# Optimization experiments

Measured on AMD Instinct MI355X. Metric: run time of the kernel, lower is better.

## Reference

```python
import jax, jax.numpy as jnp
import numpy as np

B, X, Y, Z, C = 1, 16, 16, 16, 768
NUM_HEADS = 12


def setup_inputs() -> dict:
    key = jax.random.key(0)
    k0, k1, k2 = jax.random.split(key, 3)
    x = jax.random.normal(k0, (B, X, Y, Z, C), dtype=jnp.float32)
    # Linear weights stored as [in, out] (torch stores [out, in]; math is x @ W_in_out + b)
    w_qkv = jax.random.normal(k1, (C, 3 * C), dtype=jnp.float32) * 0.02
    b_qkv = jnp.zeros((3 * C,), dtype=jnp.float32)
    w_proj = jax.random.normal(k2, (C, C), dtype=jnp.float32) * 0.02
    b_proj = jnp.zeros((C,), dtype=jnp.float32)
    return {"x": x, "w_qkv": w_qkv, "b_qkv": b_qkv, "w_proj": w_proj, "b_proj": b_proj}


def reference(x, w_qkv, b_qkv, w_proj, b_proj):
    b, xx, yy, zz, c = x.shape
    h = NUM_HEADS
    hd = c // h
    scale = hd ** (-0.5)
    n = xx * yy * zz  # flatten 3D grid into tokens

    qkv = x.reshape(b, n, c) @ w_qkv + b_qkv          # [B, N, 3C]
    qkv = qkv.reshape(b, n, 3, h, hd).transpose(2, 0, 3, 1, 4)  # [3, B, H, N, hd]
    q, k, v = qkv[0], qkv[1], qkv[2]

    attn = jnp.einsum('bhnd,bhmd->bhnm', q * scale, k)  # [B, H, N, N]
    attn = jax.nn.softmax(attn, axis=-1)
    out = jnp.einsum('bhnm,bhmd->bhnd', attn, v)        # [B, H, N, hd]
    out = out.transpose(0, 2, 1, 3).reshape(b, n, c)
    out = out @ w_proj + b_proj
    return out.reshape(b, xx, yy, zz, c)
```

## Files before the change

### kernel.cpp

```cpp
#include <hip/hip_runtime.h>
#include <cstddef>

#define N_TOK 4096
#define C_DIM 768
#define H_NUM 12
#define C3    2304
#define NSPLIT 2

typedef unsigned short u16;
using short8  = __attribute__((ext_vector_type(8))) short;
using floatx4 = __attribute__((ext_vector_type(4))) float;
using u16x4   = __attribute__((ext_vector_type(4))) u16;
using uint4v  = __attribute__((ext_vector_type(4))) unsigned;

#define K2SCALE 0.18033688011112043f

__device__ __forceinline__ u16 f2bf(float f) {
  union { float f; unsigned u; } v; v.f = f;
  unsigned r = v.u + 0x7FFFu + ((v.u >> 16) & 1u);
  return (u16)(r >> 16);
}

__device__ __forceinline__ unsigned permpack(float a, float b) {
  union { float f; unsigned u; } x, y; x.f = a; y.f = b;
  return __builtin_amdgcn_perm(y.u, x.u, 0x07060302u);
}

__device__ __forceinline__ float aexp2(float x) {
  float r;
  asm("v_exp_f32 %0, %1" : "=v"(r) : "v"(x));
  return r;
}

__device__ __forceinline__ float arcp(float x) {
  float r;
  asm("v_rcp_f32 %0, %1" : "=v"(r) : "v"(x));
  return r;
}

__device__ __forceinline__ void pl_swap32(unsigned &a, unsigned &b) {
#if __has_builtin(__builtin_amdgcn_permlane32_swap)
  auto r = __builtin_amdgcn_permlane32_swap(a, b, false, false);
  a = r[0]; b = r[1];
#else
  asm("v_permlane32_swap_b32 %0, %1" : "+v"(a), "+v"(b));
#endif
}
__device__ __forceinline__ void pl_swap16(unsigned &a, unsigned &b) {
#if __has_builtin(__builtin_amdgcn_permlane16_swap)
  auto r = __builtin_amdgcn_permlane16_swap(a, b, false, false);
  a = r[0]; b = r[1];
#else
  asm("v_permlane16_swap_b32 %0, %1" : "+v"(a), "+v"(b));
#endif
}

__device__ __forceinline__ void gload_lds16(const void* g, void* l) {
  __builtin_amdgcn_global_load_lds(
      (const __attribute__((address_space(1))) unsigned int*)g,
      (__attribute__((address_space(3))) unsigned int*)l, 16, 0, 0);
}

__global__ void k_pre(const float* __restrict__ x, u16* __restrict__ xb,
                      const float* __restrict__ wq, u16* __restrict__ wqT,
                      const float* __restrict__ wp, u16* __restrict__ wpT,
                      float* __restrict__ Oz) {
  __shared__ float tile[32][33];
  const int b = blockIdx.x;
  if (b >= 5376) {
    size_t i = (size_t)(b - 5376) * 256 + threadIdx.x;
    float4 z; z.x = 0.f; z.y = 0.f; z.z = 0.f; z.w = 0.f;
    ((float4*)Oz)[i] = z;
    return;
  }
  if (b < 3072) {
    int i = b * 256 + threadIdx.x;
    float4 f = ((const float4*)x)[i];
    u16x4 o;
    o[0] = f2bf(f.x); o[1] = f2bf(f.y); o[2] = f2bf(f.z); o[3] = f2bf(f.w);
    ((u16x4*)xb)[i] = o;
    return;
  }
  const float* in; u16* out; int Cc, bx, by;
  if (b < 4800) { int t = b - 3072; in = wq; out = wqT; Cc = 2304; bx = t % 72; by = t / 72; }
  else          { int t = b - 4800; in = wp; out = wpT; Cc = 768;  bx = t % 24; by = t / 24; }
  const int R = 768;
  const int tx = threadIdx.x & 31;
  const int ty = threadIdx.x >> 5;
  const int c0 = bx * 32, r0 = by * 32;
#pragma unroll
  for (int i = 0; i < 32; i += 8)
    tile[ty + i][tx] = in[(size_t)(r0 + ty + i) * Cc + c0 + tx];
  __syncthreads();
#pragma unroll
  for (int i = 0; i < 32; i += 8)
    out[(size_t)(c0 + ty + i) * R + r0 + tx] = f2bf(tile[tx][ty + i]);
}

__global__ __launch_bounds__(256)
void k_gemm_qkv(const u16* __restrict__ A, const u16* __restrict__ B,
                const float* __restrict__ bias, u16* __restrict__ qkv,
                u16* __restrict__ vT) {
  __shared__ u16 As[2][128 * 32];
  __shared__ u16 Bs[2][128 * 32];
  const int K = C_DIM;
  const int tid  = threadIdx.x;
  const int wave = tid >> 6, lane = tid & 63, quad = lane >> 4, l16 = lane & 15;
  const int wrow = wave >> 1, wcol = wave & 1;
  const int bm = blockIdx.y, bn = blockIdx.x;
  const int r3 = l16 & 3;

  floatx4 acc[4][4];
#pragma unroll
  for (int i = 0; i < 4; ++i)
#pragma unroll
    for (int j = 0; j < 4; ++j)
#pragma unroll
      for (int r = 0; r < 4; ++r) acc[i][j][r] = 0.f;

  const int ar = tid >> 2;
  const int ac = ((tid & 3) ^ (ar & 3)) * 8;
  const u16* gA = A + (size_t)(bm * 128 + ar) * K + ac;
  const u16* gB = B + (size_t)(bn * 128 + ar) * K + ac;

  auto stage = [&](int b, int k0) {
    gload_lds16(gA + k0,                  &As[b][tid * 8]);
    gload_lds16(gA + k0 + (size_t)64 * K, &As[b][tid * 8 + 2048]);
    gload_lds16(gB + k0,                  &Bs[b][tid * 8]);
    gload_lds16(gB + k0 + (size_t)64 * K, &Bs[b][tid * 8 + 2048]);
  };

  stage(0, 0);
  __syncthreads();
  int buf = 0;
  for (int k0 = 0; k0 < K; k0 += 32) {
    if (k0 + 32 < K) stage(buf ^ 1, k0 + 32);
    short8 af[4], bf[4];
#pragma unroll
    for (int t = 0; t < 4; ++t) {
      af[t] = *(const short8*)&As[buf][(wrow * 64 + t * 16 + l16) * 32 + ((quad ^ r3) * 8)];
      bf[t] = *(const short8*)&Bs[buf][(wcol * 64 + t * 16 + l16) * 32 + ((quad ^ r3) * 8)];
    }
#pragma unroll
    for (int tm = 0; tm < 4; ++tm)
#pragma unroll
      for (int tn = 0; tn < 4; ++tn)
        acc[tm][tn] = __builtin_amdgcn_mfma_f32_16x16x32_bf16(af[tm], bf[tn], acc[tm][tn], 0, 0, 0);
    __syncthreads();
    buf ^= 1;
  }

  const float qs = (bn < 6) ? K2SCALE : 1.0f;
#pragma unroll
  for (int tn = 0; tn < 4; ++tn) {
    const int col = bn * 128 + wcol * 64 + tn * 16 + l16;
    const float bc = bias[col];
    if (col < 1536) {
#pragma unroll
      for (int tm = 0; tm < 4; ++tm) {
        const int rowb = bm * 128 + wrow * 64 + tm * 16 + quad * 4;
#pragma unroll
        for (int r = 0; r < 4; ++r)
          qkv[(size_t)(rowb + r) * C3 + col] = f2bf((acc[tm][tn][r] + bc) * qs);
      }
    } else {
      const int hd_ = col - 1536;
#pragma unroll
      for (int tm = 0; tm < 4; ++tm) {
        const int rowb = bm * 128 + wrow * 64 + tm * 16 + quad * 4;
        u16x4 pk;
#pragma unroll
        for (int r = 0; r < 4; ++r) pk[r] = f2bf(acc[tm][tn][r] + bc);
        *(u16x4*)&vT[(size_t)hd_ * N_TOK + rowb] = pk;
      }
    }
  }
}

__global__ __launch_bounds__(256, 3)
void k_flash(const u16* __restrict__ qkv, const u16* __restrict__ vT,
             float* __restrict__ Opart, float* __restrict__ lpart) {
  __shared__ u16 Ks[2][64 * 64];
  __shared__ u16 Vs[2][64 * 64];
  const int tid  = threadIdx.x;
  const int wave = tid >> 6, lane = tid & 63, quad = lane >> 4, l16 = lane & 15;
  const int h = blockIdx.x >> 1, split = blockIdx.x & 1, qt = blockIdx.y;
  const int lr = tid >> 3;
  const int lc = ((tid & 7) ^ (lr & 7)) * 8;
  const int r7 = l16 & 7;
  const int kb = split * 2048;

  short8 bq[2][2];
#pragma unroll
  for (int qs = 0; qs < 2; ++qs)
#pragma unroll
    for (int ks = 0; ks < 2; ++ks)
      bq[qs][ks] = *(const short8*)&qkv[(size_t)(qt * 128 + wave * 32 + qs * 16 + l16) * C3
                                        + h * 64 + ks * 32 + quad * 8];

  const u16* gk = qkv + (size_t)lr * C3 + C_DIM + h * 64 + lc;
  const u16* gv = vT + (size_t)(h * 64 + lr) * N_TOK + lc;

  auto stage = [&](int b, int m0) {
#pragma unroll
    for (int p = 0; p < 2; ++p) {
      gload_lds16(gk + (size_t)(m0 + p * 32) * C3,    &Ks[b][p * 2048 + tid * 8]);
      gload_lds16(gv + (size_t)(p * 32) * N_TOK + m0, &Vs[b][p * 2048 + tid * 8]);
    }
  };

  floatx4 o0[4], o1[4], l0, l1, zv;
#pragma unroll
  for (int r = 0; r < 4; ++r) { zv[r] = 0.f; l0[r] = 0.f; l1[r] = 0.f; }
#pragma unroll
  for (int d = 0; d < 4; ++d)
#pragma unroll
    for (int r = 0; r < 4; ++r) { o0[d][r] = 0.f; o1[d][r] = 0.f; }

  short8 ones;
#pragma unroll
  for (int i = 0; i < 8; ++i) ones[i] = (short)0x3F80;

  auto compute = [&](int b) __attribute__((always_inline)) {
    const u16* kbp = &Ks[b][0];
    const u16* vb  = &Vs[b][0];
    floatx4 s0[4], s1[4];
    __builtin_amdgcn_s_setprio(1);
#pragma unroll
    for (int tn = 0; tn < 4; ++tn) {
      short8 ak = *(const short8*)&kbp[(tn * 16 + l16) * 64 + (quad ^ r7) * 8];
      s0[tn] = __builtin_amdgcn_mfma_f32_16x16x32_bf16(ak, bq[0][0], zv, 0, 0, 0);
      s1[tn] = __builtin_amdgcn_mfma_f32_16x16x32_bf16(ak, bq[1][0], zv, 0, 0, 0);
    }
#pragma unroll
    for (int tn = 0; tn < 4; ++tn) {
      short8 ak = *(const short8*)&kbp[(tn * 16 + l16) * 64 + ((quad + 4) ^ r7) * 8];
      s0[tn] = __builtin_amdgcn_mfma_f32_16x16x32_bf16(ak, bq[0][1], s0[tn], 0, 0, 0);
      s1[tn] = __builtin_amdgcn_mfma_f32_16x16x32_bf16(ak, bq[1][1], s1[tn], 0, 0, 0);
    }
    __builtin_amdgcn_s_setprio(0);

    unsigned pk0[4][2], pk1[4][2];
#pragma unroll
    for (int tn = 0; tn < 4; ++tn) {
      pk0[tn][0] = permpack(aexp2(s0[tn][0]), aexp2(s0[tn][1]));
      pk0[tn][1] = permpack(aexp2(s0[tn][2]), aexp2(s0[tn][3]));
      pk1[tn][0] = permpack(aexp2(s1[tn][0]), aexp2(s1[tn][1]));
      pk1[tn][1] = permpack(aexp2(s1[tn][2]), aexp2(s1[tn][3]));
    }
#pragma unroll
    for (int t1 = 0; t1 < 2; ++t1)
#pragma unroll
      for (int w = 0; w < 2; ++w) {
        pl_swap32(pk0[2 * t1][w], pk0[2 * t1 + 1][w]);
        pl_swap16(pk0[2 * t1][w], pk0[2 * t1 + 1][w]);
        pl_swap32(pk1[2 * t1][w], pk1[2 * t1 + 1][w]);
        pl_swap16(pk1[2 * t1][w], pk1[2 * t1 + 1][w]);
      }

#pragma unroll
    for (int ks = 0; ks < 2; ++ks) {
      uint4v t0v, t1v;
      t0v[0] = pk0[2 * ks][0]; t0v[1] = pk0[2 * ks][1];
      t0v[2] = pk0[2 * ks + 1][0]; t0v[3] = pk0[2 * ks + 1][1];
      t1v[0] = pk1[2 * ks][0]; t1v[1] = pk1[2 * ks][1];
      t1v[2] = pk1[2 * ks + 1][0]; t1v[3] = pk1[2 * ks + 1][1];
      const short8 ap0 = __builtin_bit_cast(short8, t0v);
      const short8 ap1 = __builtin_bit_cast(short8, t1v);
      __builtin_amdgcn_s_setprio(1);
#pragma unroll
      for (int dt = 0; dt < 4; ++dt) {
        short8 bv = *(const short8*)&vb[(dt * 16 + l16) * 64 + ((quad + 4 * ks) ^ r7) * 8];
        o0[dt] = __builtin_amdgcn_mfma_f32_16x16x32_bf16(ap0, bv, o0[dt], 0, 0, 0);
        o1[dt] = __builtin_amdgcn_mfma_f32_16x16x32_bf16(ap1, bv, o1[dt], 0, 0, 0);
      }
      l0 = __builtin_amdgcn_mfma_f32_16x16x32_bf16(ap0, ones, l0, 0, 0, 0);
      l1 = __builtin_amdgcn_mfma_f32_16x16x32_bf16(ap1, ones, l1, 0, 0, 0);
      __builtin_amdgcn_s_setprio(0);
    }
  };

  stage(0, kb);
  __syncthreads();
  int m0 = kb + 64;
  for (int it2 = 0; it2 < 15; ++it2) {
    stage(1, m0); m0 += 64;
    compute(0);
    __syncthreads();
    stage(0, m0); m0 += 64;
    compute(1);
    __syncthreads();
  }
  stage(1, m0);
  compute(0);
  __syncthreads();
  compute(1);

  const int rowg = qt * 128 + wave * 32 + quad * 4;
  float* Ob = Opart + (size_t)h * N_TOK * 64;
  float* lb = lpart + (size_t)h * N_TOK;
#pragma unroll
  for (int r = 0; r < 4; ++r) {
#pragma unroll
    for (int dt = 0; dt < 4; ++dt) {
      const int col = dt * 16 + l16;
      atomicAdd(&Ob[(size_t)(rowg + r) * 64 + col],      o0[dt][r]);
      atomicAdd(&Ob[(size_t)(rowg + 16 + r) * 64 + col], o1[dt][r]);
    }
    if (l16 == 0) {
      atomicAdd(&lb[rowg + r],      l0[r]);
      atomicAdd(&lb[rowg + 16 + r], l1[r]);
    }
  }
}

__global__ __launch_bounds__(256)
void k_gemm_proj(const float* __restrict__ Op, const float* __restrict__ lp,
                 const u16* __restrict__ B, const float* __restrict__ bias,
                 float* __restrict__ out) {
  __shared__ u16 As[2][64 * 32];
  __shared__ u16 Bs[2][128 * 32];
  const int K = C_DIM;
  const int tid  = threadIdx.x;
  const int wave = tid >> 6, lane = tid & 63, quad = lane >> 4, l16 = lane & 15;
  const int wrow = wave >> 1, wcol = wave & 1;
  const int bm = blockIdx.y, bn = blockIdx.x;
  const int r3 = l16 & 3;

  floatx4 acc[2][4];
#pragma unroll
  for (int i = 0; i < 2; ++i)
#pragma unroll
    for (int j = 0; j < 4; ++j)
#pragma unroll
      for (int r = 0; r < 4; ++r) acc[i][j][r] = 0.f;

  const int ar = tid >> 2;
  const int ac = ((tid & 3) ^ (ar & 3)) * 8;
  const int qrow = bm * 64 + ar;
  const u16* gB = B + (size_t)(bn * 128 + ar) * K + ac;

  auto stageA = [&](int b, int k0) {
    const int hh = k0 >> 6;
    const float rl = arcp(lp[(size_t)hh * N_TOK + qrow]);
    const float* src = &Op[((size_t)hh * N_TOK + qrow) * 64 + (k0 & 32) + ac];
    float4 v0 = *(const float4*)src;
    float4 v1 = *(const float4*)(src + 4);
    u16x4 p0, p1;
    p0[0] = f2bf(v0.x * rl); p0[1] = f2bf(v0.y * rl);
    p0[2] = f2bf(v0.z * rl); p0[3] = f2bf(v0.w * rl);
    p1[0] = f2bf(v1.x * rl); p1[1] = f2bf(v1.y * rl);
    p1[2] = f2bf(v1.z * rl); p1[3] = f2bf(v1.w * rl);
    *(u16x4*)&As[b][tid * 8]     = p0;
    *(u16x4*)&As[b][tid * 8 + 4] = p1;
  };
  auto stageB = [&](int b, int k0) {
    gload_lds16(gB + k0,                  &Bs[b][tid * 8]);
    gload_lds16(gB + k0 + (size_t)64 * K, &Bs[b][tid * 8 + 2048]);
  };

  stageB(0, 0);
  stageA(0, 0);
  __syncthreads();
  int buf = 0;
  for (int k0 = 0; k0 < K; k0 += 32) {
    if (k0 + 32 < K) { stageB(buf ^ 1, k0 + 32); stageA(buf ^ 1, k0 + 32); }
    short8 af[2], bf[4];
#pragma unroll
    for (int t = 0; t < 2; ++t)
      af[t] = *(const short8*)&As[buf][(wrow * 32 + t * 16 + l16) * 32 + ((quad ^ r3) * 8)];
#pragma unroll
    for (int t = 0; t < 4; ++t)
      bf[t] = *(const short8*)&Bs[buf][(wcol * 64 + t * 16 + l16) * 32 + ((quad ^ r3) * 8)];
#pragma unroll
    for (int tm = 0; tm < 2; ++tm)
#pragma unroll
      for (int tn = 0; tn < 4; ++tn)
        acc[tm][tn] = __builtin_amdgcn_mfma_f32_16x16x32_bf16(af[tm], bf[tn], acc[tm][tn], 0, 0, 0);
    __syncthreads();
    buf ^= 1;
  }

#pragma unroll
  for (int tn = 0; tn < 4; ++tn) {
    const int col = bn * 128 + wcol * 64 + tn * 16 + l16;
    const float bc = bias[col];
#pragma unroll
    for (int tm = 0; tm < 2; ++tm) {
      const int rowb = bm * 64 + wrow * 32 + tm * 16 + quad * 4;
#pragma unroll
      for (int r = 0; r < 4; ++r)
        out[(size_t)(rowb + r) * C_DIM + col] = acc[tm][tn][r] + bc;
    }
  }
}

extern "C" void kernel_launch(void* const* d_in, const int* in_sizes, int n_in,
                              void* d_out, int out_size, void* d_ws, size_t ws_size,
                              hipStream_t stream) {
  const float* x      = (const float*)d_in[0];
  const float* w_qkv  = (const float*)d_in[1];
  const float* b_qkv  = (const float*)d_in[2];
  const float* w_proj = (const float*)d_in[3];
  const float* b_proj = (const float*)d_in[4];
  float* out = (float*)d_out;

  u16* xb     = (u16*)d_ws;
  u16* wqkvT  = xb     + (size_t)N_TOK * C_DIM;
  u16* wprojT = wqkvT  + (size_t)C3 * C_DIM;
  u16* qkv    = wprojT + (size_t)C_DIM * C_DIM;
  u16* vT     = qkv    + (size_t)N_TOK * C3;
  float* Opart = (float*)(vT + (size_t)C_DIM * N_TOK);
  float* lpart = Opart + (size_t)H_NUM * N_TOK * 64;

  k_pre<<<8496, 256, 0, stream>>>(x, xb, w_qkv, wqkvT, w_proj, wprojT, Opart);
  k_gemm_qkv<<<dim3(C3 / 128, N_TOK / 128), 256, 0, stream>>>(xb, wqkvT, b_qkv, qkv, vT);
  k_flash<<<dim3(H_NUM * NSPLIT, N_TOK / 128), 256, 0, stream>>>(qkv, vT, Opart, lpart);
  k_gemm_proj<<<dim3(C_DIM / 128, N_TOK / 64), 256, 0, stream>>>(Opart, lpart, wprojT, b_proj, out);
}
```

Baseline: 192.1 us.

## Replace split-KV atomics with per-split partial buffers and swap grid block order

The flash kernel now writes each KV split's partial output and row-sum into its own buffer with plain stores, where it previously used atomicAdd into a shared accumulator. The projection GEMM sums the two partials when it loads its A tile. This removes the zero-fill blocks in the preprocessing kernel and the atomic traffic, at the cost of twice the partial-buffer memory and extra reads in the projection. The grid x/y mapping of both GEMMs is also swapped so that consecutive blocks walk along M instead of N, which changes cache reuse.

```diff
diff --git a/kernel.cpp b/kernel.cpp
--- a/kernel.cpp
+++ b/kernel.cpp
@@ -63,16 +63,9 @@
 
 __global__ void k_pre(const float* __restrict__ x, u16* __restrict__ xb,
                       const float* __restrict__ wq, u16* __restrict__ wqT,
-                      const float* __restrict__ wp, u16* __restrict__ wpT,
-                      float* __restrict__ Oz) {
+                      const float* __restrict__ wp, u16* __restrict__ wpT) {
   __shared__ float tile[32][33];
   const int b = blockIdx.x;
-  if (b >= 5376) {
-    size_t i = (size_t)(b - 5376) * 256 + threadIdx.x;
-    float4 z; z.x = 0.f; z.y = 0.f; z.z = 0.f; z.w = 0.f;
-    ((float4*)Oz)[i] = z;
-    return;
-  }
   if (b < 3072) {
     int i = b * 256 + threadIdx.x;
     float4 f = ((const float4*)x)[i];
@@ -107,7 +100,7 @@
   const int tid  = threadIdx.x;
   const int wave = tid >> 6, lane = tid & 63, quad = lane >> 4, l16 = lane & 15;
   const int wrow = wave >> 1, wcol = wave & 1;
-  const int bm = blockIdx.y, bn = blockIdx.x;
+  const int bm = blockIdx.x, bn = blockIdx.y;
   const int r3 = l16 & 3;
 
   floatx4 acc[4][4];
@@ -297,19 +290,19 @@
   compute(1);
 
   const int rowg = qt * 128 + wave * 32 + quad * 4;
-  float* Ob = Opart + (size_t)h * N_TOK * 64;
-  float* lb = lpart + (size_t)h * N_TOK;
+  float* Ob = Opart + (size_t)(split * H_NUM + h) * N_TOK * 64;
+  float* lb = lpart + (size_t)(split * H_NUM + h) * N_TOK;
 #pragma unroll
   for (int r = 0; r < 4; ++r) {
 #pragma unroll
     for (int dt = 0; dt < 4; ++dt) {
       const int col = dt * 16 + l16;
-      atomicAdd(&Ob[(size_t)(rowg + r) * 64 + col],      o0[dt][r]);
-      atomicAdd(&Ob[(size_t)(rowg + 16 + r) * 64 + col], o1[dt][r]);
+      Ob[(size_t)(rowg + r) * 64 + col]      = o0[dt][r];
+      Ob[(size_t)(rowg + 16 + r) * 64 + col] = o1[dt][r];
     }
     if (l16 == 0) {
-      atomicAdd(&lb[rowg + r],      l0[r]);
-      atomicAdd(&lb[rowg + 16 + r], l1[r]);
+      lb[rowg + r]      = l0[r];
+      lb[rowg + 16 + r] = l1[r];
     }
   }
 }
@@ -321,10 +314,12 @@
   __shared__ u16 As[2][64 * 32];
   __shared__ u16 Bs[2][128 * 32];
   const int K = C_DIM;
+  const size_t OSTRIDE = (size_t)H_NUM * N_TOK * 64;
+  const size_t LSTRIDE = (size_t)H_NUM * N_TOK;
   const int tid  = threadIdx.x;
   const int wave = tid >> 6, lane = tid & 63, quad = lane >> 4, l16 = lane & 15;
   const int wrow = wave >> 1, wcol = wave & 1;
-  const int bm = blockIdx.y, bn = blockIdx.x;
+  const int bm = blockIdx.x, bn = blockIdx.y;
   const int r3 = l16 & 3;
 
   floatx4 acc[2][4];
@@ -342,15 +337,19 @@
 
   auto stageA = [&](int b, int k0) {
     const int hh = k0 >> 6;
-    const float rl = arcp(lp[(size_t)hh * N_TOK + qrow]);
-    const float* src = &Op[((size_t)hh * N_TOK + qrow) * 64 + (k0 & 32) + ac];
-    float4 v0 = *(const float4*)src;
-    float4 v1 = *(const float4*)(src + 4);
+    const size_t rowi = (size_t)hh * N_TOK + qrow;
+    const float rl = arcp(lp[rowi] + lp[rowi + LSTRIDE]);
+    const float* s0 = &Op[rowi * 64 + (k0 & 32) + ac];
+    const float* s1 = s0 + OSTRIDE;
+    float4 a0 = *(const float4*)s0;
+    float4 a1 = *(const float4*)(s0 + 4);
+    float4 b0 = *(const float4*)s1;
+    float4 b1 = *(const float4*)(s1 + 4);
     u16x4 p0, p1;
-    p0[0] = f2bf(v0.x * rl); p0[1] = f2bf(v0.y * rl);
-    p0[2] = f2bf(v0.z * rl); p0[3] = f2bf(v0.w * rl);
-    p1[0] = f2bf(v1.x * rl); p1[1] = f2bf(v1.y * rl);
-    p1[2] = f2bf(v1.z * rl); p1[3] = f2bf(v1.w * rl);
+    p0[0] = f2bf((a0.x + b0.x) * rl); p0[1] = f2bf((a0.y + b0.y) * rl);
+    p0[2] = f2bf((a0.z + b0.z) * rl); p0[3] = f2bf((a0.w + b0.w) * rl);
+    p1[0] = f2bf((a1.x + b1.x) * rl); p1[1] = f2bf((a1.y + b1.y) * rl);
+    p1[2] = f2bf((a1.z + b1.z) * rl); p1[3] = f2bf((a1.w + b1.w) * rl);
     *(u16x4*)&As[b][tid * 8]     = p0;
     *(u16x4*)&As[b][tid * 8 + 4] = p1;
   };
@@ -411,10 +410,10 @@
   u16* qkv    = wprojT + (size_t)C_DIM * C_DIM;
   u16* vT     = qkv    + (size_t)N_TOK * C3;
   float* Opart = (float*)(vT + (size_t)C_DIM * N_TOK);
-  float* lpart = Opart + (size_t)H_NUM * N_TOK * 64;
-
-  k_pre<<<8496, 256, 0, stream>>>(x, xb, w_qkv, wqkvT, w_proj, wprojT, Opart);
-  k_gemm_qkv<<<dim3(C3 / 128, N_TOK / 128), 256, 0, stream>>>(xb, wqkvT, b_qkv, qkv, vT);
+  float* lpart = Opart + (size_t)NSPLIT * H_NUM * N_TOK * 64;
+
+  k_pre<<<5376, 256, 0, stream>>>(x, xb, w_qkv, wqkvT, w_proj, wprojT);
+  k_gemm_qkv<<<dim3(N_TOK / 128, C3 / 128), 256, 0, stream>>>(xb, wqkvT, b_qkv, qkv, vT);
   k_flash<<<dim3(H_NUM * NSPLIT, N_TOK / 128), 256, 0, stream>>>(qkv, vT, Opart, lpart);
-  k_gemm_proj<<<dim3(C_DIM / 128, N_TOK / 64), 256, 0, stream>>>(Opart, lpart, wprojT, b_proj, out);
-}
+  k_gemm_proj<<<dim3(N_TOK / 64, C_DIM / 128), 256, 0, stream>>>(Opart, lpart, wprojT, b_proj, out);
+}
```

Measured after the change: 180.8 us, median of 3. -5.9%, faster.
